# Performance work log

Measured on AMD Instinct MI355X. Metric: run time of the kernel, lower is better.

Reference implementation:

```python
import jax, jax.numpy as jnp
import numpy as np

N_NODES = 100000
N_EDGES = 1600000
IN_FEATS = 512
OUT_FEATS = 64


def setup_inputs() -> dict:
    key = jax.random.key(0)
    k1, k2, k3, k4, k5 = jax.random.split(key, 5)
    feat = jax.random.normal(k1, (N_NODES, IN_FEATS), dtype=jnp.float32)
    edge_src = jax.random.randint(k2, (N_EDGES,), 0, N_NODES, dtype=jnp.int32)
    edge_dst = jax.random.randint(k3, (N_EDGES,), 0, N_NODES, dtype=jnp.int32)
    edge_w = jax.random.uniform(k4, (N_EDGES,), dtype=jnp.float32)
    # xavier_uniform init for weight [in, out]
    limit = float(np.sqrt(6.0 / (IN_FEATS + OUT_FEATS)))
    weight = jax.random.uniform(k5, (IN_FEATS, OUT_FEATS), dtype=jnp.float32,
                                minval=-limit, maxval=limit)
    bias = jnp.zeros((OUT_FEATS,), dtype=jnp.float32)
    return {"feat": feat, "edge_w": edge_w, "weight": weight, "bias": bias,
            "edge_src": edge_src, "edge_dst": edge_dst}


def reference(feat, edge_w, weight, bias, edge_src, edge_dst):
    # in_feats (512) > out_feats (64): project first, then message/aggregate.
    h = jnp.matmul(feat, weight)                     # [N, out]
    m = h[edge_src] * edge_w[:, None]                # u_mul_e: [E, out]
    msum = jax.ops.segment_sum(m, edge_dst, num_segments=N_NODES)   # [N, out]
    deg = jax.ops.segment_sum(jnp.ones_like(edge_w), edge_dst,
                              num_segments=N_NODES)                  # [N]
    # mean reduce; zero in-degree nodes get 0 (DGL mean semantics)
    rst = jnp.where(deg[:, None] > 0, msum / jnp.maximum(deg, 1.0)[:, None], 0.0)
    rst = rst + bias
    return jax.nn.relu(rst)
```

## Files before the change

kernel.cpp:

```cpp
#include <hip/hip_runtime.h>

#define N_NODES 100000
#define N_EDGES 1600000
#define IN_F 512
#define OUT_F 64

#define NBINS 391
#define K3_CHUNK 4096
#define K3_BLOCKS ((N_EDGES + K3_CHUNK - 1) / K3_CHUNK)
#define CAP 6144

typedef __bf16 bf16_t;
typedef bf16_t bf16x8 __attribute__((ext_vector_type(8)));
typedef float f32x4 __attribute__((ext_vector_type(4)));

__device__ __forceinline__ unsigned short f2bf(float f) {
    unsigned int u = __float_as_uint(f);
    u += 0x7FFFu + ((u >> 16) & 1u);
    return (unsigned short)(u >> 16);
}
__device__ __forceinline__ float bf2f(unsigned short s) {
    return __uint_as_float((unsigned int)s << 16);
}

__global__ __launch_bounds__(256) void prep_wt(const float* __restrict__ W,
                                               unsigned short* __restrict__ Wt,
                                               int* __restrict__ gcursor) {
    const int i = blockIdx.x * 256 + threadIdx.x;
    const int k = i >> 6, n = i & 63;
    Wt[(size_t)n * IN_F + k] = f2bf(W[i]);
    if (i < 512) gcursor[i] = i * CAP;
}

__global__ __launch_bounds__(256) void gemm_direct(const float* __restrict__ A,
                                                   const unsigned short* __restrict__ Wt,
                                                   unsigned short* __restrict__ H) {
    const int t = threadIdx.x;
    const int lane = t & 63;
    const int w = t >> 6;
    const int arow = lane & 15;
    const int kk = (lane >> 4) << 3;

    const float* ap[2];
    #pragma unroll
    for (int rf = 0; rf < 2; ++rf) {
        int r = blockIdx.x * 128 + (w << 5) + (rf << 4) + arow;
        if (r >= N_NODES) r = N_NODES - 1;
        ap[rf] = A + (size_t)r * IN_F + kk;
    }

    f32x4 acc[2][4];
    #pragma unroll
    for (int i = 0; i < 2; ++i)
        #pragma unroll
        for (int j = 0; j < 4; ++j)
            acc[i][j] = (f32x4){0.f, 0.f, 0.f, 0.f};

    float4 nxt[2][2];
    #pragma unroll
    for (int rf = 0; rf < 2; ++rf) {
        nxt[rf][0] = *(const float4*)(ap[rf] + 0);
        nxt[rf][1] = *(const float4*)(ap[rf] + 4);
    }

    for (int k0 = 0; k0 < IN_F; k0 += 32) {
        float4 cur[2][2];
        #pragma unroll
        for (int rf = 0; rf < 2; ++rf) {
            cur[rf][0] = nxt[rf][0];
            cur[rf][1] = nxt[rf][1];
        }
        if (k0 + 32 < IN_F) {
            #pragma unroll
            for (int rf = 0; rf < 2; ++rf) {
                nxt[rf][0] = *(const float4*)(ap[rf] + k0 + 32);
                nxt[rf][1] = *(const float4*)(ap[rf] + k0 + 36);
            }
        }

        bf16x8 afrag[2];
        #pragma unroll
        for (int rf = 0; rf < 2; ++rf) {
            bf16x8 af;
            af[0] = (bf16_t)cur[rf][0].x; af[1] = (bf16_t)cur[rf][0].y;
            af[2] = (bf16_t)cur[rf][0].z; af[3] = (bf16_t)cur[rf][0].w;
            af[4] = (bf16_t)cur[rf][1].x; af[5] = (bf16_t)cur[rf][1].y;
            af[6] = (bf16_t)cur[rf][1].z; af[7] = (bf16_t)cur[rf][1].w;
            afrag[rf] = af;
        }

        bf16x8 bfrag[4];
        #pragma unroll
        for (int cf = 0; cf < 4; ++cf) {
            const int col = (cf << 4) + arow;
            bfrag[cf] = *(const bf16x8*)(Wt + (size_t)col * IN_F + k0 + kk);
        }

        #pragma unroll
        for (int rf = 0; rf < 2; ++rf)
            #pragma unroll
            for (int cf = 0; cf < 4; ++cf)
                acc[rf][cf] = __builtin_amdgcn_mfma_f32_16x16x32_bf16(
                    afrag[rf], bfrag[cf], acc[rf][cf], 0, 0, 0);
    }

    #pragma unroll
    for (int rf = 0; rf < 2; ++rf) {
        const int rbase = blockIdx.x * 128 + (w << 5) + (rf << 4) + ((lane >> 4) << 2);
        #pragma unroll
        for (int j = 0; j < 4; ++j) {
            const int row = rbase + j;
            if (row < N_NODES) {
                #pragma unroll
                for (int cf = 0; cf < 4; ++cf) {
                    const int col = (cf << 4) + arow;
                    H[(size_t)row * OUT_F + col] = f2bf(acc[rf][cf][j]);
                }
            }
        }
    }
}

__global__ __launch_bounds__(512) void scatter_coarse(const int* __restrict__ esrc,
                                                      const int* __restrict__ edst,
                                                      const float* __restrict__ ew,
                                                      int* __restrict__ gcursor,
                                                      int2* __restrict__ meta) {
    __shared__ int hist[NBINS];
    __shared__ int base[NBINS];
    __shared__ int binstart[NBINS];
    __shared__ int lcur[NBINS];
    __shared__ int wsum[8];
    __shared__ int2 sorted[K3_CHUNK];
    __shared__ unsigned short binof[K3_CHUNK];

    const int t = threadIdx.x;
    const int wv = t >> 6, ln = t & 63;
    const int e0 = blockIdx.x * K3_CHUNK;

    for (int i = t; i < NBINS; i += 512) { hist[i] = 0; lcur[i] = 0; }
    __syncthreads();

    int2 ed[8];
    int  bins[8];
    #pragma unroll
    for (int i = 0; i < 8; ++i) {
        const int e = e0 + i * 512 + t;
        if (e < N_EDGES) {
            const int s = esrc[e];
            const int d = edst[e];
            bins[i] = d >> 8;
            ed[i] = make_int2(s | ((d & 255) << 17), __float_as_int(ew[e]));
            atomicAdd(&hist[bins[i]], 1);
        } else {
            bins[i] = -1;
        }
    }
    __syncthreads();

    const int v = (t < NBINS) ? hist[t] : 0;
    int x = v;
    #pragma unroll
    for (int off = 1; off < 64; off <<= 1) {
        const int y = __shfl_up(x, off, 64);
        if (ln >= off) x += y;
    }
    if (ln == 63) wsum[wv] = x;
    __syncthreads();
    int pre = 0, tot = 0;
    #pragma unroll
    for (int k = 0; k < 8; ++k) {
        const int s = wsum[k];
        if (k < wv) pre += s;
        tot += s;
    }
    x += pre;
    if (t < NBINS) {
        binstart[t] = x - v;
        base[t] = (v > 0) ? atomicAdd(&gcursor[t], v) : 0;
    }
    __syncthreads();

    #pragma unroll
    for (int i = 0; i < 8; ++i) {
        if (bins[i] >= 0) {
            const int r = atomicAdd(&lcur[bins[i]], 1);
            const int slot = binstart[bins[i]] + r;
            sorted[slot] = ed[i];
            binof[slot] = (unsigned short)bins[i];
        }
    }
    __syncthreads();

    for (int s = t; s < tot; s += 512) {
        const int b = binof[s];
        meta[base[b] + (s - binstart[b])] = sorted[s];
    }
}

__global__ __launch_bounds__(512) void fine_sort(const int2* __restrict__ meta,
                                                 const int* __restrict__ gcursor,
                                                 unsigned int* __restrict__ meta2,
                                                 int* __restrict__ start,
                                                 int* __restrict__ counts) {
    __shared__ int hist[256];
    __shared__ int scn[256];
    __shared__ int cur[256];
    __shared__ int ws4[4];
    __shared__ unsigned int sorted[CAP];

    const int b = blockIdx.x;
    const int t = threadIdx.x;
    const int wv = t >> 6, ln = t & 63;
    const size_t s0 = (size_t)b * CAP;
    int cnt = gcursor[b] - b * CAP;
    if (cnt > CAP) cnt = CAP;

    if (t < 256) { hist[t] = 0; cur[t] = 0; }
    __syncthreads();

    for (int i = t; i < cnt; i += 512)
        atomicAdd(&hist[(meta[s0 + i].x >> 17) & 255], 1);
    __syncthreads();

    const int v = (t < 256) ? hist[t] : 0;
    int x = v;
    #pragma unroll
    for (int off = 1; off < 64; off <<= 1) {
        const int y = __shfl_up(x, off, 64);
        if (ln >= off) x += y;
    }
    if (t < 256 && ln == 63) ws4[wv] = x;
    __syncthreads();
    if (t < 256) {
        int pre = 0;
        #pragma unroll
        for (int k = 0; k < 4; ++k) if (k < wv) pre += ws4[k];
        scn[t] = x + pre;
    }
    __syncthreads();

    for (int i = t; i < cnt; i += 512) {
        const int2 m = meta[s0 + i];
        const int ld = (m.x >> 17) & 255;
        const unsigned int wb = f2bf(__int_as_float(m.y));
        const unsigned int p = (unsigned int)(m.x & 0x1FFFF) | (wb << 17);
        const int r = atomicAdd(&cur[ld], 1);
        sorted[(scn[ld] - hist[ld]) + r] = p;
    }
    __syncthreads();

    for (int i = t; i < cnt; i += 512) meta2[s0 + i] = sorted[i];
    const int node0 = b << 8;
    if (t < 256 && node0 + t < N_NODES) {
        counts[node0 + t] = hist[t];
        start[node0 + t]  = (int)s0 + scn[t] - hist[t];
    }
}

__global__ __launch_bounds__(256) void aggregate_kernel(const unsigned short* __restrict__ h,
                                                        const int* __restrict__ start,
                                                        const int* __restrict__ counts,
                                                        const unsigned int* __restrict__ meta,
                                                        const float* __restrict__ bias,
                                                        float* __restrict__ out) {
    const int wave = threadIdx.x >> 6;
    const int lane = threadIdx.x & 63;
    const int n0 = blockIdx.x * 16 + wave * 4;
    const int g = lane & 15;

    int s[4], c[4];
    #pragma unroll
    for (int q = 0; q < 4; ++q) { s[q] = start[n0 + q]; c[q] = counts[n0 + q]; }

    float acc[4] = {0.f, 0.f, 0.f, 0.f};
    int maxc = c[0];
    #pragma unroll
    for (int q = 1; q < 4; ++q) maxc = max(maxc, c[q]);

    for (int b = 0; b < maxc; b += 16) {
        unsigned int m[4];
        #pragma unroll
        for (int q = 0; q < 4; ++q)
            m[q] = (g < c[q] - b) ? meta[(size_t)s[q] + b + g] : 0u;
        #pragma unroll
        for (int j = 0; j < 16; ++j) {
            #pragma unroll
            for (int q = 0; q < 4; ++q) {
                const unsigned int p = __shfl(m[q], j, 16);
                const int   src = (int)(p & 0x1FFFF);
                const float wv  = __uint_as_float((p >> 17) << 16);
                acc[q] = fmaf(bf2f(h[(size_t)src * OUT_F + lane]), wv, acc[q]);
            }
        }
    }

    const float bv = bias[lane];
    #pragma unroll
    for (int q = 0; q < 4; ++q) {
        const float r = (c[q] > 0) ? (acc[q] / (float)c[q]) : 0.f;
        out[(size_t)(n0 + q) * OUT_F + lane] = fmaxf(r + bv, 0.f);
    }
}

extern "C" void kernel_launch(void* const* d_in, const int* in_sizes, int n_in,
                              void* d_out, int out_size, void* d_ws, size_t ws_size,
                              hipStream_t stream) {
    const float* feat   = (const float*)d_in[0];
    const float* edge_w = (const float*)d_in[1];
    const float* weight = (const float*)d_in[2];
    const float* bias   = (const float*)d_in[3];
    const int*   esrc   = (const int*)d_in[4];
    const int*   edst   = (const int*)d_in[5];

    float* out = (float*)d_out;

    char* ws = (char*)d_ws;
    int2*           meta  = (int2*)ws;            ws += (size_t)NBINS * CAP * 8;
    unsigned int*   meta2 = (unsigned int*)ws;    ws += (size_t)NBINS * CAP * 4;
    unsigned short* h     = (unsigned short*)ws;  ws += (size_t)N_NODES * OUT_F * 2;
    unsigned short* Wt    = (unsigned short*)ws;  ws += (size_t)OUT_F * IN_F * 2;
    int* counts  = (int*)ws;  ws += (size_t)N_NODES * 4;
    int* start   = (int*)ws;  ws += (size_t)N_NODES * 4;
    int* gcursor = (int*)ws;  ws += 512 * 4;

    prep_wt<<<(IN_F * OUT_F) / 256, 256, 0, stream>>>(weight, Wt, gcursor);
    scatter_coarse<<<K3_BLOCKS, 512, 0, stream>>>(esrc, edst, edge_w, gcursor, meta);
    fine_sort<<<NBINS, 512, 0, stream>>>(meta, gcursor, meta2, start, counts);
    gemm_direct<<<(N_NODES + 127) / 128, 256, 0, stream>>>(feat, Wt, h);
    aggregate_kernel<<<N_NODES / 16, 256, 0, stream>>>(h, start, counts,
                                                       meta2, bias, out);
}
```

Measured before the change: 141.7 us.

## Deepen GEMM prefetch, enlarge scatter chunks, and give each aggregate wave more nodes

The GEMM now prefetches 64 K-elements per step instead of 32, which doubles the loads in flight per iteration. The coarse scatter handles 6144 edges per block and drops the per-slot bin array; each slot's bin is instead found by a binary search over the bin starts. The aggregate kernel processes 8 nodes per wave instead of 4, so more gather loads are in flight. The costs are higher register pressure in the GEMM and aggregate kernels, extra search work in the scatter, and fewer blocks in flight overall.

```diff
diff --git a/kernel.cpp b/kernel.cpp
--- a/kernel.cpp
+++ b/kernel.cpp
@@ -6,8 +6,9 @@
 #define OUT_F 64
 
 #define NBINS 391
-#define K3_CHUNK 4096
+#define K3_CHUNK 6144
 #define K3_BLOCKS ((N_EDGES + K3_CHUNK - 1) / K3_CHUNK)
+#define K3_PER_T (K3_CHUNK / 512)
 #define CAP 6144
 
 typedef __bf16 bf16_t;
@@ -56,52 +57,80 @@
         for (int j = 0; j < 4; ++j)
             acc[i][j] = (f32x4){0.f, 0.f, 0.f, 0.f};
 
-    float4 nxt[2][2];
+    float4 nxt[2][4];
     #pragma unroll
     for (int rf = 0; rf < 2; ++rf) {
         nxt[rf][0] = *(const float4*)(ap[rf] + 0);
         nxt[rf][1] = *(const float4*)(ap[rf] + 4);
-    }
-
-    for (int k0 = 0; k0 < IN_F; k0 += 32) {
-        float4 cur[2][2];
-        #pragma unroll
-        for (int rf = 0; rf < 2; ++rf) {
-            cur[rf][0] = nxt[rf][0];
-            cur[rf][1] = nxt[rf][1];
-        }
-        if (k0 + 32 < IN_F) {
+        nxt[rf][2] = *(const float4*)(ap[rf] + 32);
+        nxt[rf][3] = *(const float4*)(ap[rf] + 36);
+    }
+
+    for (int k0 = 0; k0 < IN_F; k0 += 64) {
+        float4 cur[2][4];
+        #pragma unroll
+        for (int rf = 0; rf < 2; ++rf)
+            #pragma unroll
+            for (int q = 0; q < 4; ++q) cur[rf][q] = nxt[rf][q];
+
+        if (k0 + 64 < IN_F) {
             #pragma unroll
             for (int rf = 0; rf < 2; ++rf) {
-                nxt[rf][0] = *(const float4*)(ap[rf] + k0 + 32);
-                nxt[rf][1] = *(const float4*)(ap[rf] + k0 + 36);
-            }
-        }
-
-        bf16x8 afrag[2];
-        #pragma unroll
-        for (int rf = 0; rf < 2; ++rf) {
-            bf16x8 af;
-            af[0] = (bf16_t)cur[rf][0].x; af[1] = (bf16_t)cur[rf][0].y;
-            af[2] = (bf16_t)cur[rf][0].z; af[3] = (bf16_t)cur[rf][0].w;
-            af[4] = (bf16_t)cur[rf][1].x; af[5] = (bf16_t)cur[rf][1].y;
-            af[6] = (bf16_t)cur[rf][1].z; af[7] = (bf16_t)cur[rf][1].w;
-            afrag[rf] = af;
-        }
-
-        bf16x8 bfrag[4];
-        #pragma unroll
-        for (int cf = 0; cf < 4; ++cf) {
-            const int col = (cf << 4) + arow;
-            bfrag[cf] = *(const bf16x8*)(Wt + (size_t)col * IN_F + k0 + kk);
-        }
-
-        #pragma unroll
-        for (int rf = 0; rf < 2; ++rf)
-            #pragma unroll
-            for (int cf = 0; cf < 4; ++cf)
-                acc[rf][cf] = __builtin_amdgcn_mfma_f32_16x16x32_bf16(
-                    afrag[rf], bfrag[cf], acc[rf][cf], 0, 0, 0);
+                nxt[rf][0] = *(const float4*)(ap[rf] + k0 + 64);
+                nxt[rf][1] = *(const float4*)(ap[rf] + k0 + 68);
+                nxt[rf][2] = *(const float4*)(ap[rf] + k0 + 96);
+                nxt[rf][3] = *(const float4*)(ap[rf] + k0 + 100);
+            }
+        }
+
+        {
+            bf16x8 afrag[2];
+            #pragma unroll
+            for (int rf = 0; rf < 2; ++rf) {
+                bf16x8 af;
+                af[0] = (bf16_t)cur[rf][0].x; af[1] = (bf16_t)cur[rf][0].y;
+                af[2] = (bf16_t)cur[rf][0].z; af[3] = (bf16_t)cur[rf][0].w;
+                af[4] = (bf16_t)cur[rf][1].x; af[5] = (bf16_t)cur[rf][1].y;
+                af[6] = (bf16_t)cur[rf][1].z; af[7] = (bf16_t)cur[rf][1].w;
+                afrag[rf] = af;
+            }
+            bf16x8 bfrag[4];
+            #pragma unroll
+            for (int cf = 0; cf < 4; ++cf) {
+                const int col = (cf << 4) + arow;
+                bfrag[cf] = *(const bf16x8*)(Wt + (size_t)col * IN_F + k0 + kk);
+            }
+            #pragma unroll
+            for (int rf = 0; rf < 2; ++rf)
+                #pragma unroll
+                for (int cf = 0; cf < 4; ++cf)
+                    acc[rf][cf] = __builtin_amdgcn_mfma_f32_16x16x32_bf16(
+                        afrag[rf], bfrag[cf], acc[rf][cf], 0, 0, 0);
+        }
+        {
+            bf16x8 afrag[2];
+            #pragma unroll
+            for (int rf = 0; rf < 2; ++rf) {
+                bf16x8 af;
+                af[0] = (bf16_t)cur[rf][2].x; af[1] = (bf16_t)cur[rf][2].y;
+                af[2] = (bf16_t)cur[rf][2].z; af[3] = (bf16_t)cur[rf][2].w;
+                af[4] = (bf16_t)cur[rf][3].x; af[5] = (bf16_t)cur[rf][3].y;
+                af[6] = (bf16_t)cur[rf][3].z; af[7] = (bf16_t)cur[rf][3].w;
+                afrag[rf] = af;
+            }
+            bf16x8 bfrag[4];
+            #pragma unroll
+            for (int cf = 0; cf < 4; ++cf) {
+                const int col = (cf << 4) + arow;
+                bfrag[cf] = *(const bf16x8*)(Wt + (size_t)col * IN_F + k0 + 32 + kk);
+            }
+            #pragma unroll
+            for (int rf = 0; rf < 2; ++rf)
+                #pragma unroll
+                for (int cf = 0; cf < 4; ++cf)
+                    acc[rf][cf] = __builtin_amdgcn_mfma_f32_16x16x32_bf16(
+                        afrag[rf], bfrag[cf], acc[rf][cf], 0, 0, 0);
+        }
     }
 
     #pragma unroll
@@ -128,23 +157,23 @@
                                                       int2* __restrict__ meta) {
     __shared__ int hist[NBINS];
     __shared__ int base[NBINS];
-    __shared__ int binstart[NBINS];
+    __shared__ int binstart[512];
     __shared__ int lcur[NBINS];
     __shared__ int wsum[8];
     __shared__ int2 sorted[K3_CHUNK];
-    __shared__ unsigned short binof[K3_CHUNK];
 
     const int t = threadIdx.x;
     const int wv = t >> 6, ln = t & 63;
     const int e0 = blockIdx.x * K3_CHUNK;
 
     for (int i = t; i < NBINS; i += 512) { hist[i] = 0; lcur[i] = 0; }
-    __syncthreads();
-
-    int2 ed[8];
-    int  bins[8];
-    #pragma unroll
-    for (int i = 0; i < 8; ++i) {
+    if (t >= NBINS) binstart[t] = 0x7FFFFFFF;
+    __syncthreads();
+
+    int2 ed[K3_PER_T];
+    int  bins[K3_PER_T];
+    #pragma unroll
+    for (int i = 0; i < K3_PER_T; ++i) {
         const int e = e0 + i * 512 + t;
         if (e < N_EDGES) {
             const int s = esrc[e];
@@ -182,19 +211,22 @@
     __syncthreads();
 
     #pragma unroll
-    for (int i = 0; i < 8; ++i) {
+    for (int i = 0; i < K3_PER_T; ++i) {
         if (bins[i] >= 0) {
             const int r = atomicAdd(&lcur[bins[i]], 1);
-            const int slot = binstart[bins[i]] + r;
-            sorted[slot] = ed[i];
-            binof[slot] = (unsigned short)bins[i];
+            sorted[binstart[bins[i]] + r] = ed[i];
         }
     }
     __syncthreads();
 
     for (int s = t; s < tot; s += 512) {
-        const int b = binof[s];
-        meta[base[b] + (s - binstart[b])] = sorted[s];
+        int lo = 0;
+        #pragma unroll
+        for (int step = 256; step > 0; step >>= 1) {
+            const int cand = lo + step;
+            if (cand < 512 && binstart[cand] <= s) lo = cand;
+        }
+        meta[base[lo] + (s - binstart[lo])] = sorted[s];
     }
 }
 
@@ -266,27 +298,27 @@
                                                         float* __restrict__ out) {
     const int wave = threadIdx.x >> 6;
     const int lane = threadIdx.x & 63;
-    const int n0 = blockIdx.x * 16 + wave * 4;
+    const int n0 = blockIdx.x * 32 + wave * 8;
     const int g = lane & 15;
 
-    int s[4], c[4];
-    #pragma unroll
-    for (int q = 0; q < 4; ++q) { s[q] = start[n0 + q]; c[q] = counts[n0 + q]; }
-
-    float acc[4] = {0.f, 0.f, 0.f, 0.f};
+    int s[8], c[8];
+    #pragma unroll
+    for (int q = 0; q < 8; ++q) { s[q] = start[n0 + q]; c[q] = counts[n0 + q]; }
+
+    float acc[8] = {0.f, 0.f, 0.f, 0.f, 0.f, 0.f, 0.f, 0.f};
     int maxc = c[0];
     #pragma unroll
-    for (int q = 1; q < 4; ++q) maxc = max(maxc, c[q]);
+    for (int q = 1; q < 8; ++q) maxc = max(maxc, c[q]);
 
     for (int b = 0; b < maxc; b += 16) {
-        unsigned int m[4];
-        #pragma unroll
-        for (int q = 0; q < 4; ++q)
+        unsigned int m[8];
+        #pragma unroll
+        for (int q = 0; q < 8; ++q)
             m[q] = (g < c[q] - b) ? meta[(size_t)s[q] + b + g] : 0u;
         #pragma unroll
         for (int j = 0; j < 16; ++j) {
             #pragma unroll
-            for (int q = 0; q < 4; ++q) {
+            for (int q = 0; q < 8; ++q) {
                 const unsigned int p = __shfl(m[q], j, 16);
                 const int   src = (int)(p & 0x1FFFF);
                 const float wv  = __uint_as_float((p >> 17) << 16);
@@ -297,7 +329,7 @@
 
     const float bv = bias[lane];
     #pragma unroll
-    for (int q = 0; q < 4; ++q) {
+    for (int q = 0; q < 8; ++q) {
         const float r = (c[q] > 0) ? (acc[q] / (float)c[q]) : 0.f;
         out[(size_t)(n0 + q) * OUT_F + lane] = fmaxf(r + bv, 0.f);
     }
@@ -328,6 +360,6 @@
     scatter_coarse<<<K3_BLOCKS, 512, 0, stream>>>(esrc, edst, edge_w, gcursor, meta);
     fine_sort<<<NBINS, 512, 0, stream>>>(meta, gcursor, meta2, start, counts);
     gemm_direct<<<(N_NODES + 127) / 128, 256, 0, stream>>>(feat, Wt, h);
-    aggregate_kernel<<<N_NODES / 16, 256, 0, stream>>>(h, start, counts,
+    aggregate_kernel<<<N_NODES / 32, 256, 0, stream>>>(h, start, counts,
                                                        meta2, bias, out);
 }
```

Result: slower. 174.4 us (+23.1%).
